# Performance work log

Hardware: AMD Instinct MI355X
Metric: run time of the kernel (lower is better)

## Reference

```python
import jax, jax.numpy as jnp
import numpy as np

B, T, D, H = 4, 1024, 1024, 16
DK = D // H
SCALE = float(np.sqrt(DK))


def setup_inputs() -> dict:
    key = jax.random.key(0)
    ks = jax.random.split(key, 12)
    std = 1.0 / np.sqrt(D)
    inp = {
        "x": jax.random.normal(ks[0], (B, T, D), dtype=jnp.float32),
        "s2_distances": jax.random.uniform(ks[1], (B, T, T), dtype=jnp.float32),
        # causal mask: 1 where attention allowed (j <= i)
        "mask": jnp.broadcast_to(jnp.tril(jnp.ones((T, T), dtype=jnp.int32)), (B, T, T)),
        "Wq": jax.random.uniform(ks[2], (D, D), jnp.float32, -std, std),
        "bq": jax.random.uniform(ks[3], (D,), jnp.float32, -std, std),
        "Wk": jax.random.uniform(ks[4], (D, D), jnp.float32, -std, std),
        "bk": jax.random.uniform(ks[5], (D,), jnp.float32, -std, std),
        "Wv": jax.random.uniform(ks[6], (D, D), jnp.float32, -std, std),
        "bv": jax.random.uniform(ks[7], (D,), jnp.float32, -std, std),
        "Wo": jax.random.uniform(ks[8], (D, D), jnp.float32, -std, std),
        "bo": jax.random.uniform(ks[9], (D,), jnp.float32, -std, std),
        "spatial_weight": jnp.float32(0.5),
    }
    return inp


def reference(x, s2_distances, mask, Wq, bq, Wk, bk, Wv, bv, Wo, bo, spatial_weight):
    b, t, _ = x.shape
    # projections: torch nn.Linear is x @ W.T + b
    def proj(W, bias):
        y = jnp.einsum("btd,ed->bte", x, W) + bias
        return y.reshape(b, t, H, DK).transpose(0, 2, 1, 3)  # [B,H,T,dk]

    Q, K, V = proj(Wq, bq), proj(Wk, bk), proj(Wv, bv)
    # scores: QK^T/sqrt(dk) - |alpha| * dist  (dist broadcast over heads)
    scores = jnp.einsum("bhqd,bhkd->bhqk", Q, K) / SCALE
    scores = scores - jnp.abs(spatial_weight) * s2_distances[:, None, :, :]
    scores = jnp.where(mask[:, None, :, :] == 0, -jnp.inf, scores)
    probs = jax.nn.softmax(scores, axis=-1)
    out = jnp.einsum("bhqk,bhkd->bhqd", probs, V)
    out = out.transpose(0, 2, 1, 3).reshape(b, t, D)
    return jnp.einsum("btd,ed->bte", out, Wo) + bo
```

## Files before the change

### kernel.cpp

```cpp
#include <hip/hip_runtime.h>
#include <stdint.h>

#define Tt 1024
#define Dd 1024
#define Hh 16

typedef unsigned short u16;
typedef __attribute__((ext_vector_type(8))) short short8;
typedef __attribute__((ext_vector_type(4))) float f32x4;
typedef __attribute__((ext_vector_type(4))) unsigned short u16x4;

typedef const __attribute__((address_space(1))) uint32_t* gptr_t;
typedef __attribute__((address_space(3))) uint32_t* lptr_t;

#define QSCALE 0.18033688011112042f
#define LOG2E 1.4426950408889634f

static __device__ __forceinline__ u16 f2bf(float f) {
  union { float f; unsigned u; } x;
  x.f = f;
  unsigned u = x.u;
  return (u16)((u + 0x7fffu + ((u >> 16) & 1u)) >> 16);
}

static __device__ __forceinline__ u16 f2bf_fast(float f) {
  union { float f; unsigned u; } x;
  x.f = f;
  return (u16)((x.u + 0x8000u) >> 16);
}

static __device__ __forceinline__ float fexp2(float x) {
#if __has_builtin(__builtin_amdgcn_exp2f)
  return __builtin_amdgcn_exp2f(x);
#else
  return exp2f(x);
#endif
}

__global__ __launch_bounds__(256) void cvt_kernel(
    const float* __restrict__ x, const float* __restrict__ wq,
    const float* __restrict__ wk, const float* __restrict__ wv,
    const float* __restrict__ wo, u16* __restrict__ xb, u16* __restrict__ wb) {
  size_t i = ((size_t)blockIdx.x * 256 + threadIdx.x) * 4;
  const size_t XN = (size_t)4 * 1024 * 1024;
  const float* src;
  u16* dst;
  size_t off;
  if (i < XN) {
    src = x; dst = xb; off = i;
  } else {
    size_t j = i - XN;
    int wi = (int)(j >> 20);
    src = (wi == 0) ? wq : (wi == 1) ? wk : (wi == 2) ? wv : wo;
    dst = wb + ((size_t)wi << 20);
    off = j & ((1u << 20) - 1);
  }
  float4 v = *(const float4*)(src + off);
  u16x4 o;
  o.x = f2bf(v.x); o.y = f2bf(v.y); o.z = f2bf(v.z); o.w = f2bf(v.w);
  *(u16x4*)(dst + off) = o;
}

static __device__ __forceinline__ void gemm_mainloop_db(
    const u16* __restrict__ A, const u16* __restrict__ W,
    u16* lds, int m0, int n0, f32x4 acc[2][4]) {
  const int t = threadIdx.x;
  const int w = t >> 6, l = t & 63;
  const int quad = l >> 4, l15 = l & 15;
  const int wm = (w >> 1) * 32, wn = (w & 1) * 64;
  const int srow = t >> 3;
  const int scol = ((l & 7) ^ ((l >> 3) & 7)) * 8;
  const u16* ga = A + (size_t)(m0 + srow) * Dd + scol;
  const u16* gb = W + (size_t)(n0 + srow) * Dd + scol;
  char* ldc = (char*)lds;
  const int xr = l15 & 7;

  auto stage = [&](int k0, int buf) {
    char* base = ldc + buf * 32768 + w * 1024;
#pragma unroll
    for (int i = 0; i < 2; i++) {
      __builtin_amdgcn_global_load_lds((gptr_t)(ga + k0 + (size_t)i * 64 * Dd),
                                       (lptr_t)(base + i * 8192), 16, 0, 0);
      __builtin_amdgcn_global_load_lds((gptr_t)(gb + k0 + (size_t)i * 64 * Dd),
                                       (lptr_t)(base + 16384 + i * 8192), 16, 0, 0);
    }
  };

  stage(0, 0);
#pragma unroll 1
  for (int it = 0; it < Dd / 64; it++) {
    const int buf = it & 1;
    __builtin_amdgcn_s_waitcnt(0);
    __syncthreads();
    if (it + 1 < Dd / 64) stage((it + 1) * 64, buf ^ 1);
    const u16* lA = lds + buf * 16384;
    const u16* lB = lA + 8192;
#pragma unroll
    for (int kk = 0; kk < 2; kk++) {
      short8 af[2], bfr[4];
#pragma unroll
      for (int mi = 0; mi < 2; mi++)
        af[mi] = *(const short8*)(lA + (wm + mi * 16 + l15) * 64 +
                                  (((kk * 4 + quad) ^ xr) * 8));
#pragma unroll
      for (int ni = 0; ni < 4; ni++)
        bfr[ni] = *(const short8*)(lB + (wn + ni * 16 + l15) * 64 +
                                   (((kk * 4 + quad) ^ xr) * 8));
#pragma unroll
      for (int mi = 0; mi < 2; mi++)
#pragma unroll
        for (int ni = 0; ni < 4; ni++)
          acc[mi][ni] = __builtin_amdgcn_mfma_f32_16x16x32_bf16(af[mi], bfr[ni], acc[mi][ni], 0, 0, 0);
    }
  }
}

__global__ __launch_bounds__(512) void gemm_qkv_kernel(
    const u16* __restrict__ xb, const u16* __restrict__ wb,
    const float* __restrict__ bq, const float* __restrict__ bk,
    const float* __restrict__ bv, u16* __restrict__ Q, u16* __restrict__ Kk,
    u16* __restrict__ Vt) {
  __shared__ u16 lds[2 * 16384];
  const int z = blockIdx.z;
  const u16* W = wb + ((size_t)z << 20);
  const float* bias = (z == 0) ? bq : (z == 1) ? bk : bv;
  const int m0 = blockIdx.x * 128, n0 = blockIdx.y * 128;
  f32x4 acc[2][4];
#pragma unroll
  for (int i = 0; i < 2; i++)
#pragma unroll
    for (int j = 0; j < 4; j++) acc[i][j] = (f32x4){0.f, 0.f, 0.f, 0.f};
  gemm_mainloop_db(xb, W, lds, m0, n0, acc);
  const int t = threadIdx.x, w = t >> 6, l = t & 63, quad = l >> 4, l15 = l & 15;
  const int wm = (w >> 1) * 32, wn = (w & 1) * 64;
  u16* smem = lds;
  __syncthreads();
  const float scl = (z == 0) ? QSCALE : 1.0f;
  if (z < 2) {
#pragma unroll
    for (int mi = 0; mi < 2; mi++)
#pragma unroll
      for (int ni = 0; ni < 4; ni++) {
        const int n = wn + ni * 16 + l15;
        const float bn = bias[n0 + n];
#pragma unroll
        for (int r = 0; r < 4; r++) {
          const int m = wm + mi * 16 + quad * 4 + r;
          smem[m * 128 + n] = f2bf((acc[mi][ni][r] + bn) * scl);
        }
      }
  } else {
#pragma unroll
    for (int mi = 0; mi < 2; mi++)
#pragma unroll
      for (int ni = 0; ni < 4; ni++) {
        const int n = wn + ni * 16 + l15;
        const float bn = bias[n0 + n];
        u16x4 o;
        o.x = f2bf(acc[mi][ni][0] + bn);
        o.y = f2bf(acc[mi][ni][1] + bn);
        o.z = f2bf(acc[mi][ni][2] + bn);
        o.w = f2bf(acc[mi][ni][3] + bn);
        *(u16x4*)&smem[n * 128 + wm + mi * 16 + quad * 4] = o;
      }
  }
  __syncthreads();
  const int row = t >> 4;
  const int col = (t & 15) * 8;
  if (z < 2) {
    u16* out = (z == 0) ? Q : Kk;
#pragma unroll
    for (int it = 0; it < 4; it++) {
      const int rr = it * 32 + row;
      *(short8*)(out + (size_t)(m0 + rr) * Dd + n0 + col) = *(const short8*)&smem[rr * 128 + col];
    }
  } else {
    const int b2 = m0 >> 10, tt0 = m0 & (Tt - 1);
#pragma unroll
    for (int it = 0; it < 4; it++) {
      const int rr = it * 32 + row;
      *(short8*)(Vt + ((size_t)b2 * Dd + n0 + rr) * Tt + tt0 + col) = *(const short8*)&smem[rr * 128 + col];
    }
  }
}

__global__ __launch_bounds__(512) void gemm_out_kernel(
    const u16* __restrict__ Ao, const u16* __restrict__ Wo,
    const float* __restrict__ bo, float* __restrict__ out) {
  __shared__ u16 lds[2 * 16384];
  const int m0 = blockIdx.x * 128, n0 = blockIdx.y * 128;
  f32x4 acc[2][4];
#pragma unroll
  for (int i = 0; i < 2; i++)
#pragma unroll
    for (int j = 0; j < 4; j++) acc[i][j] = (f32x4){0.f, 0.f, 0.f, 0.f};
  gemm_mainloop_db(Ao, Wo, lds, m0, n0, acc);
  const int t = threadIdx.x, w = t >> 6, l = t & 63, quad = l >> 4, l15 = l & 15;
  const int wm = (w >> 1) * 32, wn = (w & 1) * 64;
#pragma unroll
  for (int mi = 0; mi < 2; mi++)
#pragma unroll
    for (int ni = 0; ni < 4; ni++) {
      const int n = n0 + wn + ni * 16 + l15;
      const float bn = bo[n];
#pragma unroll
      for (int r = 0; r < 4; r++) {
        const int m = m0 + wm + mi * 16 + quad * 4 + r;
        out[(size_t)m * Dd + n] = acc[mi][ni][r] + bn;
      }
    }
}

__global__ __launch_bounds__(256) void attn_kernel(
    const u16* __restrict__ Q, const u16* __restrict__ Kk,
    const u16* __restrict__ Vt, const float* __restrict__ dist,
    const float* __restrict__ alphap, u16* __restrict__ Oo) {
  __shared__ u16 lK[2][64 * 64];
  __shared__ u16 lV[2][64 * 64];
  __shared__ u16 lPp[4][16 * 64];
  const int t = threadIdx.x, w = t >> 6, l = t & 63, quad = l >> 4, l15 = l & 15;
  const int pi = blockIdx.x & 7;
  const int bh = blockIdx.x >> 3;
  const int h = bh & (Hh - 1), b = bh >> 4;
  const int qbA = pi, qbB = 15 - pi;
  const float aL = fabsf(alphap[0]) * LOG2E;
  const float* distb = dist + (size_t)b * Tt * Tt;

  const int srow = w * 8 + (l >> 3);
  const int schunk = ((l & 7) ^ ((l >> 3) & 7)) * 8;
  const u16* gK = Kk + ((size_t)b * Tt + srow) * Dd + h * 64 + schunk;
  const u16* gV = Vt + ((size_t)b * Dd + h * 64 + srow) * Tt + schunk;
  char* lKc0 = (char*)&lK[0][0];
  char* lVc0 = (char*)&lV[0][0];
  const int wbase = w * 1024;

  auto stage = [&](int k0, int buf) {
#pragma unroll
    for (int i = 0; i < 2; i++) {
      __builtin_amdgcn_global_load_lds(
          (gptr_t)(gK + (size_t)(k0 + i * 32) * Dd),
          (lptr_t)(lKc0 + buf * 8192 + wbase + i * 4096), 16, 0, 0);
      __builtin_amdgcn_global_load_lds(
          (gptr_t)(gV + (size_t)(i * 32) * Tt + k0),
          (lptr_t)(lVc0 + buf * 8192 + wbase + i * 4096), 16, 0, 0);
    }
  };

  const int qrowA = qbA * 64 + w * 16 + l15;
  const int qrowB = qbB * 64 + w * 16 + l15;
  const u16* QpA = Q + ((size_t)b * Tt + qrowA) * Dd + h * 64 + quad * 8;
  const u16* QpB = Q + ((size_t)b * Tt + qrowB) * Dd + h * 64 + quad * 8;
  const short8 qfA0 = *(const short8*)QpA;
  const short8 qfA1 = *(const short8*)(QpA + 32);
  const short8 qfB0 = *(const short8*)QpB;
  const short8 qfB1 = *(const short8*)(QpB + 32);
  const float* dpA = distb + (size_t)qrowA * Tt + quad * 4;
  const float* dpB = distb + (size_t)qrowB * Tt + quad * 4;

  const int xr = l15 & 7;
  u16* lpr = &lPp[w][l15 * 64];

  f32x4 ddA[4], ddB[4];
  stage(0, 0);
#pragma unroll
  for (int nt = 0; nt < 4; nt++) ddA[nt] = *(const f32x4*)(dpA + nt * 16);

  int gi = 0;
#pragma unroll 1
  for (int half = 0; half < 2; half++) {
    const int qb = half ? qbB : qbA;
    const int q0 = qb * 64;
    const int niter = qb + 1;
    const short8 qf0 = half ? qfB0 : qfA0;
    const short8 qf1 = half ? qfB1 : qfA1;
    const float* dp = half ? dpB : dpA;
    const int qrow = half ? qrowB : qrowA;
    f32x4 oacc[4];
#pragma unroll
    for (int dt = 0; dt < 4; dt++) oacc[dt] = (f32x4){0.f, 0.f, 0.f, 0.f};
    float lsum = 0.f;

#pragma unroll 1
    for (int kt = 0; kt < niter; kt++, gi++) {
      const int buf = gi & 1;
      __builtin_amdgcn_s_waitcnt(0);
      __syncthreads();
      const bool more = (kt + 1 < niter);
      if (more) {
        stage((kt + 1) * 64, buf ^ 1);
#pragma unroll
        for (int nt = 0; nt < 4; nt++)
          ddB[nt] = *(const f32x4*)(dp + (kt + 1) * 64 + nt * 16);
      } else if (half == 0) {
        stage(0, buf ^ 1);
#pragma unroll
        for (int nt = 0; nt < 4; nt++) ddB[nt] = *(const f32x4*)(dpB + nt * 16);
      }
      f32x4 sacc[4];
#pragma unroll
      for (int nt = 0; nt < 4; nt++) {
#pragma unroll
        for (int r = 0; r < 4; r++) sacc[nt][r] = -aL * ddA[nt][r];
      }
#pragma unroll
      for (int ks = 0; ks < 2; ks++) {
        const short8 qf = ks ? qf1 : qf0;
        const int cs = ((ks * 4 + quad) ^ xr) * 8;
#pragma unroll
        for (int nt = 0; nt < 4; nt++) {
          const short8 kf = *(const short8*)&lK[buf][(nt * 16 + l15) * 64 + cs];
          sacc[nt] = __builtin_amdgcn_mfma_f32_16x16x32_bf16(kf, qf, sacc[nt], 0, 0, 0);
        }
      }
      if (kt == qb) {
        const int kbase = kt * 64 + quad * 4;
#pragma unroll
        for (int nt = 0; nt < 4; nt++) {
          u16x4 pk;
#pragma unroll
          for (int r = 0; r < 4; r++) {
            const float p = (kbase + nt * 16 + r <= qrow) ? fexp2(sacc[nt][r]) : 0.f;
            lsum += p;
            pk[r] = f2bf_fast(p);
          }
          *(u16x4*)&lpr[((nt * 4 + quad) ^ (xr << 1)) * 4] = pk;
        }
      } else {
#pragma unroll
        for (int nt = 0; nt < 4; nt++) {
          u16x4 pk;
#pragma unroll
          for (int r = 0; r < 4; r++) {
            const float p = fexp2(sacc[nt][r]);
            lsum += p;
            pk[r] = f2bf_fast(p);
          }
          *(u16x4*)&lpr[((nt * 4 + quad) ^ (xr << 1)) * 4] = pk;
        }
      }
#pragma unroll
      for (int ks = 0; ks < 2; ks++) {
        const short8 pa = *(const short8*)&lpr[((ks * 4 + quad) ^ xr) * 8];
        const int cs = ((ks * 4 + quad) ^ xr) * 8;
#pragma unroll
        for (int dt = 0; dt < 4; dt++) {
          const short8 vf = *(const short8*)&lV[buf][(dt * 16 + l15) * 64 + cs];
          oacc[dt] = __builtin_amdgcn_mfma_f32_16x16x32_bf16(pa, vf, oacc[dt], 0, 0, 0);
        }
      }
#pragma unroll
      for (int nt = 0; nt < 4; nt++) ddA[nt] = ddB[nt];
    }

    lsum += __shfl_xor(lsum, 16);
    lsum += __shfl_xor(lsum, 32);
    const float inv = 1.0f / lsum;
    float invq[4];
#pragma unroll
    for (int r = 0; r < 4; r++) invq[r] = __shfl(inv, quad * 4 + r);
#pragma unroll
    for (int dt = 0; dt < 4; dt++) {
#pragma unroll
      for (int r = 0; r < 4; r++) {
        Oo[((size_t)b * Tt + q0 + w * 16 + quad * 4 + r) * Dd + h * 64 + dt * 16 + l15] =
            f2bf(oacc[dt][r] * invq[r]);
      }
    }
  }
}

extern "C" void kernel_launch(void* const* d_in, const int* in_sizes, int n_in,
                              void* d_out, int out_size, void* d_ws, size_t ws_size,
                              hipStream_t stream) {
  const float* x = (const float*)d_in[0];
  const float* dist = (const float*)d_in[1];
  const float* Wq = (const float*)d_in[3];
  const float* bq = (const float*)d_in[4];
  const float* Wk = (const float*)d_in[5];
  const float* bk = (const float*)d_in[6];
  const float* Wv = (const float*)d_in[7];
  const float* bv = (const float*)d_in[8];
  const float* Wo = (const float*)d_in[9];
  const float* bo = (const float*)d_in[10];
  const float* alphap = (const float*)d_in[11];

  char* ws = (char*)d_ws;
  u16* xb = (u16*)(ws);
  u16* wb = (u16*)(ws + ((size_t)8 << 20));
  u16* Qb = (u16*)(ws + ((size_t)16 << 20));
  u16* Kb = (u16*)(ws + ((size_t)24 << 20));
  u16* Vtb = (u16*)(ws + ((size_t)32 << 20));
  u16* Ob = xb;
  float* outp = (float*)d_out;

  cvt_kernel<<<8192, 256, 0, stream>>>(x, Wq, Wk, Wv, Wo, xb, wb);
  dim3 g1(32, 8, 3);
  gemm_qkv_kernel<<<g1, 512, 0, stream>>>(xb, wb, bq, bk, bv, Qb, Kb, Vtb);
  attn_kernel<<<512, 256, 0, stream>>>(Qb, Kb, Vtb, dist, alphap, Ob);
  dim3 g2(32, 8);
  gemm_out_kernel<<<g2, 512, 0, stream>>>(Ob, wb + ((size_t)3 << 20), bo, outp);
}
```

Baseline: 196.6 us.

## Prescale distance bias to bf16, split attention blocks per q-tile, narrow out-proj tiles

The convert kernel now also turns the full distance matrix into a bf16 bias already multiplied by -|alpha|*log2e, so the attention kernel streams half as many bytes and skips the per-element multiply. The attention grid changes from paired q-blocks (balanced causal work) to one q-block per workgroup, with the largest blocks dispatched first, doubling the block count. The output projection uses 128x64 tiles with its own inline mainloop, giving twice as many blocks for better CU fill. The cost is an extra full read and write of the distance matrix in the convert pass, plus bf16 rounding of the bias.

After: 197.0 us. About the same (+0.2%).

```diff
diff --git a/kernel.cpp b/kernel.cpp
--- a/kernel.cpp
+++ b/kernel.cpp
@@ -27,6 +27,12 @@
   union { float f; unsigned u; } x;
   x.f = f;
   return (u16)((x.u + 0x8000u) >> 16);
+}
+
+static __device__ __forceinline__ float bf2f(u16 u) {
+  union { unsigned u; float f; } x;
+  x.u = ((unsigned)u) << 16;
+  return x.f;
 }
 
 static __device__ __forceinline__ float fexp2(float x) {
@@ -40,24 +46,32 @@
 __global__ __launch_bounds__(256) void cvt_kernel(
     const float* __restrict__ x, const float* __restrict__ wq,
     const float* __restrict__ wk, const float* __restrict__ wv,
-    const float* __restrict__ wo, u16* __restrict__ xb, u16* __restrict__ wb) {
+    const float* __restrict__ wo, const float* __restrict__ dist,
+    const float* __restrict__ alphap, u16* __restrict__ xb,
+    u16* __restrict__ wb, u16* __restrict__ biasb) {
   size_t i = ((size_t)blockIdx.x * 256 + threadIdx.x) * 4;
   const size_t XN = (size_t)4 * 1024 * 1024;
+  const size_t WN = (size_t)4 * 1024 * 1024;
+  float scl = 1.0f;
   const float* src;
   u16* dst;
   size_t off;
   if (i < XN) {
     src = x; dst = xb; off = i;
-  } else {
+  } else if (i < XN + WN) {
     size_t j = i - XN;
     int wi = (int)(j >> 20);
     src = (wi == 0) ? wq : (wi == 1) ? wk : (wi == 2) ? wv : wo;
     dst = wb + ((size_t)wi << 20);
     off = j & ((1u << 20) - 1);
+  } else {
+    src = dist; dst = biasb; off = i - XN - WN;
+    scl = -fabsf(alphap[0]) * LOG2E;
   }
   float4 v = *(const float4*)(src + off);
   u16x4 o;
-  o.x = f2bf(v.x); o.y = f2bf(v.y); o.z = f2bf(v.z); o.w = f2bf(v.w);
+  o.x = f2bf(v.x * scl); o.y = f2bf(v.y * scl);
+  o.z = f2bf(v.z * scl); o.w = f2bf(v.w * scl);
   *(u16x4*)(dst + off) = o;
 }
 
@@ -187,44 +201,73 @@
 __global__ __launch_bounds__(512) void gemm_out_kernel(
     const u16* __restrict__ Ao, const u16* __restrict__ Wo,
     const float* __restrict__ bo, float* __restrict__ out) {
-  __shared__ u16 lds[2 * 16384];
-  const int m0 = blockIdx.x * 128, n0 = blockIdx.y * 128;
-  f32x4 acc[2][4];
-#pragma unroll
-  for (int i = 0; i < 2; i++)
-#pragma unroll
-    for (int j = 0; j < 4; j++) acc[i][j] = (f32x4){0.f, 0.f, 0.f, 0.f};
-  gemm_mainloop_db(Ao, Wo, lds, m0, n0, acc);
+  __shared__ u16 lds[2 * 12288];
+  const int m0 = blockIdx.x * 128, n0 = blockIdx.y * 64;
   const int t = threadIdx.x, w = t >> 6, l = t & 63, quad = l >> 4, l15 = l & 15;
-  const int wm = (w >> 1) * 32, wn = (w & 1) * 64;
-#pragma unroll
-  for (int mi = 0; mi < 2; mi++)
-#pragma unroll
-    for (int ni = 0; ni < 4; ni++) {
-      const int n = n0 + wn + ni * 16 + l15;
-      const float bn = bo[n];
-#pragma unroll
-      for (int r = 0; r < 4; r++) {
-        const int m = m0 + wm + mi * 16 + quad * 4 + r;
-        out[(size_t)m * Dd + n] = acc[mi][ni][r] + bn;
-      }
-    }
+  const int srow = t >> 3;
+  const int scol = ((l & 7) ^ ((l >> 3) & 7)) * 8;
+  const u16* ga = Ao + (size_t)(m0 + srow) * Dd + scol;
+  const u16* gb = Wo + (size_t)(n0 + srow) * Dd + scol;
+  char* ldc = (char*)lds;
+  const int xr = l15 & 7;
+  f32x4 acc[4];
+#pragma unroll
+  for (int j = 0; j < 4; j++) acc[j] = (f32x4){0.f, 0.f, 0.f, 0.f};
+
+  auto stage = [&](int k0, int buf) {
+    char* base = ldc + buf * 24576 + w * 1024;
+#pragma unroll
+    for (int i = 0; i < 2; i++)
+      __builtin_amdgcn_global_load_lds((gptr_t)(ga + k0 + (size_t)i * 64 * Dd),
+                                       (lptr_t)(base + i * 8192), 16, 0, 0);
+    __builtin_amdgcn_global_load_lds((gptr_t)(gb + k0),
+                                     (lptr_t)(base + 16384), 16, 0, 0);
+  };
+
+  stage(0, 0);
+#pragma unroll 1
+  for (int it = 0; it < Dd / 64; it++) {
+    const int buf = it & 1;
+    __builtin_amdgcn_s_waitcnt(0);
+    __syncthreads();
+    if (it + 1 < Dd / 64) stage((it + 1) * 64, buf ^ 1);
+    const u16* lA = lds + buf * 12288;
+    const u16* lB = lA + 8192;
+#pragma unroll
+    for (int kk = 0; kk < 2; kk++) {
+      const int cs = ((kk * 4 + quad) ^ xr) * 8;
+      const short8 af = *(const short8*)(lA + (w * 16 + l15) * 64 + cs);
+#pragma unroll
+      for (int ni = 0; ni < 4; ni++) {
+        const short8 bfr = *(const short8*)(lB + (ni * 16 + l15) * 64 + cs);
+        acc[ni] = __builtin_amdgcn_mfma_f32_16x16x32_bf16(af, bfr, acc[ni], 0, 0, 0);
+      }
+    }
+  }
+#pragma unroll
+  for (int ni = 0; ni < 4; ni++) {
+    const int n = n0 + ni * 16 + l15;
+    const float bn = bo[n];
+#pragma unroll
+    for (int r = 0; r < 4; r++) {
+      const int m = m0 + w * 16 + quad * 4 + r;
+      out[(size_t)m * Dd + n] = acc[ni][r] + bn;
+    }
+  }
 }
 
 __global__ __launch_bounds__(256) void attn_kernel(
     const u16* __restrict__ Q, const u16* __restrict__ Kk,
-    const u16* __restrict__ Vt, const float* __restrict__ dist,
-    const float* __restrict__ alphap, u16* __restrict__ Oo) {
+    const u16* __restrict__ Vt, const u16* __restrict__ biasb,
+    u16* __restrict__ Oo) {
   __shared__ u16 lK[2][64 * 64];
   __shared__ u16 lV[2][64 * 64];
   __shared__ u16 lPp[4][16 * 64];
   const int t = threadIdx.x, w = t >> 6, l = t & 63, quad = l >> 4, l15 = l & 15;
-  const int pi = blockIdx.x & 7;
-  const int bh = blockIdx.x >> 3;
+  const int qb = 15 - (blockIdx.x >> 6);
+  const int bh = blockIdx.x & 63;
   const int h = bh & (Hh - 1), b = bh >> 4;
-  const int qbA = pi, qbB = 15 - pi;
-  const float aL = fabsf(alphap[0]) * LOG2E;
-  const float* distb = dist + (size_t)b * Tt * Tt;
+  const int q0 = qb * 64;
 
   const int srow = w * 8 + (l >> 3);
   const int schunk = ((l & 7) ^ ((l >> 3) & 7)) * 8;
@@ -246,125 +289,105 @@
     }
   };
 
-  const int qrowA = qbA * 64 + w * 16 + l15;
-  const int qrowB = qbB * 64 + w * 16 + l15;
-  const u16* QpA = Q + ((size_t)b * Tt + qrowA) * Dd + h * 64 + quad * 8;
-  const u16* QpB = Q + ((size_t)b * Tt + qrowB) * Dd + h * 64 + quad * 8;
-  const short8 qfA0 = *(const short8*)QpA;
-  const short8 qfA1 = *(const short8*)(QpA + 32);
-  const short8 qfB0 = *(const short8*)QpB;
-  const short8 qfB1 = *(const short8*)(QpB + 32);
-  const float* dpA = distb + (size_t)qrowA * Tt + quad * 4;
-  const float* dpB = distb + (size_t)qrowB * Tt + quad * 4;
+  const int qrow = q0 + w * 16 + l15;
+  const u16* Qp = Q + ((size_t)b * Tt + qrow) * Dd + h * 64 + quad * 8;
+  const short8 qf0 = *(const short8*)Qp;
+  const short8 qf1 = *(const short8*)(Qp + 32);
+  const u16* bp = biasb + ((size_t)b * Tt + qrow) * Tt + quad * 4;
 
   const int xr = l15 & 7;
   u16* lpr = &lPp[w][l15 * 64];
-
-  f32x4 ddA[4], ddB[4];
+  const int niter = qb + 1;
+
+  f32x4 oacc[4];
+#pragma unroll
+  for (int dt = 0; dt < 4; dt++) oacc[dt] = (f32x4){0.f, 0.f, 0.f, 0.f};
+  float lsum = 0.f;
+  u16x4 bbA[4], bbB[4];
+
   stage(0, 0);
 #pragma unroll
-  for (int nt = 0; nt < 4; nt++) ddA[nt] = *(const f32x4*)(dpA + nt * 16);
-
-  int gi = 0;
+  for (int nt = 0; nt < 4; nt++) bbA[nt] = *(const u16x4*)(bp + nt * 16);
+
 #pragma unroll 1
-  for (int half = 0; half < 2; half++) {
-    const int qb = half ? qbB : qbA;
-    const int q0 = qb * 64;
-    const int niter = qb + 1;
-    const short8 qf0 = half ? qfB0 : qfA0;
-    const short8 qf1 = half ? qfB1 : qfA1;
-    const float* dp = half ? dpB : dpA;
-    const int qrow = half ? qrowB : qrowA;
-    f32x4 oacc[4];
-#pragma unroll
-    for (int dt = 0; dt < 4; dt++) oacc[dt] = (f32x4){0.f, 0.f, 0.f, 0.f};
-    float lsum = 0.f;
-
-#pragma unroll 1
-    for (int kt = 0; kt < niter; kt++, gi++) {
-      const int buf = gi & 1;
-      __builtin_amdgcn_s_waitcnt(0);
-      __syncthreads();
-      const bool more = (kt + 1 < niter);
-      if (more) {
-        stage((kt + 1) * 64, buf ^ 1);
-#pragma unroll
-        for (int nt = 0; nt < 4; nt++)
-          ddB[nt] = *(const f32x4*)(dp + (kt + 1) * 64 + nt * 16);
-      } else if (half == 0) {
-        stage(0, buf ^ 1);
-#pragma unroll
-        for (int nt = 0; nt < 4; nt++) ddB[nt] = *(const f32x4*)(dpB + nt * 16);
-      }
-      f32x4 sacc[4];
+  for (int kt = 0; kt < niter; kt++) {
+    const int buf = kt & 1;
+    __builtin_amdgcn_s_waitcnt(0);
+    __syncthreads();
+    if (kt + 1 < niter) {
+      stage((kt + 1) * 64, buf ^ 1);
+#pragma unroll
+      for (int nt = 0; nt < 4; nt++)
+        bbB[nt] = *(const u16x4*)(bp + (kt + 1) * 64 + nt * 16);
+    }
+    f32x4 sacc[4];
+#pragma unroll
+    for (int nt = 0; nt < 4; nt++) {
+#pragma unroll
+      for (int r = 0; r < 4; r++) sacc[nt][r] = bf2f(bbA[nt][r]);
+    }
+#pragma unroll
+    for (int ks = 0; ks < 2; ks++) {
+      const short8 qf = ks ? qf1 : qf0;
+      const int cs = ((ks * 4 + quad) ^ xr) * 8;
 #pragma unroll
       for (int nt = 0; nt < 4; nt++) {
-#pragma unroll
-        for (int r = 0; r < 4; r++) sacc[nt][r] = -aL * ddA[nt][r];
-      }
-#pragma unroll
-      for (int ks = 0; ks < 2; ks++) {
-        const short8 qf = ks ? qf1 : qf0;
-        const int cs = ((ks * 4 + quad) ^ xr) * 8;
-#pragma unroll
-        for (int nt = 0; nt < 4; nt++) {
-          const short8 kf = *(const short8*)&lK[buf][(nt * 16 + l15) * 64 + cs];
-          sacc[nt] = __builtin_amdgcn_mfma_f32_16x16x32_bf16(kf, qf, sacc[nt], 0, 0, 0);
+        const short8 kf = *(const short8*)&lK[buf][(nt * 16 + l15) * 64 + cs];
+        sacc[nt] = __builtin_amdgcn_mfma_f32_16x16x32_bf16(kf, qf, sacc[nt], 0, 0, 0);
+      }
+    }
+    if (kt == qb) {
+      const int kbase = kt * 64 + quad * 4;
+#pragma unroll
+      for (int nt = 0; nt < 4; nt++) {
+        u16x4 pk;
+#pragma unroll
+        for (int r = 0; r < 4; r++) {
+          const float p = (kbase + nt * 16 + r <= qrow) ? fexp2(sacc[nt][r]) : 0.f;
+          lsum += p;
+          pk[r] = f2bf_fast(p);
         }
-      }
-      if (kt == qb) {
-        const int kbase = kt * 64 + quad * 4;
-#pragma unroll
-        for (int nt = 0; nt < 4; nt++) {
-          u16x4 pk;
-#pragma unroll
-          for (int r = 0; r < 4; r++) {
-            const float p = (kbase + nt * 16 + r <= qrow) ? fexp2(sacc[nt][r]) : 0.f;
-            lsum += p;
-            pk[r] = f2bf_fast(p);
-          }
-          *(u16x4*)&lpr[((nt * 4 + quad) ^ (xr << 1)) * 4] = pk;
+        *(u16x4*)&lpr[((nt * 4 + quad) ^ (xr << 1)) * 4] = pk;
+      }
+    } else {
+#pragma unroll
+      for (int nt = 0; nt < 4; nt++) {
+        u16x4 pk;
+#pragma unroll
+        for (int r = 0; r < 4; r++) {
+          const float p = fexp2(sacc[nt][r]);
+          lsum += p;
+          pk[r] = f2bf_fast(p);
         }
-      } else {
-#pragma unroll
-        for (int nt = 0; nt < 4; nt++) {
-          u16x4 pk;
-#pragma unroll
-          for (int r = 0; r < 4; r++) {
-            const float p = fexp2(sacc[nt][r]);
-            lsum += p;
-            pk[r] = f2bf_fast(p);
-          }
-          *(u16x4*)&lpr[((nt * 4 + quad) ^ (xr << 1)) * 4] = pk;
-        }
-      }
-#pragma unroll
-      for (int ks = 0; ks < 2; ks++) {
-        const short8 pa = *(const short8*)&lpr[((ks * 4 + quad) ^ xr) * 8];
-        const int cs = ((ks * 4 + quad) ^ xr) * 8;
-#pragma unroll
-        for (int dt = 0; dt < 4; dt++) {
-          const short8 vf = *(const short8*)&lV[buf][(dt * 16 + l15) * 64 + cs];
-          oacc[dt] = __builtin_amdgcn_mfma_f32_16x16x32_bf16(pa, vf, oacc[dt], 0, 0, 0);
-        }
-      }
-#pragma unroll
-      for (int nt = 0; nt < 4; nt++) ddA[nt] = ddB[nt];
-    }
-
-    lsum += __shfl_xor(lsum, 16);
-    lsum += __shfl_xor(lsum, 32);
-    const float inv = 1.0f / lsum;
-    float invq[4];
-#pragma unroll
-    for (int r = 0; r < 4; r++) invq[r] = __shfl(inv, quad * 4 + r);
-#pragma unroll
-    for (int dt = 0; dt < 4; dt++) {
-#pragma unroll
-      for (int r = 0; r < 4; r++) {
-        Oo[((size_t)b * Tt + q0 + w * 16 + quad * 4 + r) * Dd + h * 64 + dt * 16 + l15] =
-            f2bf(oacc[dt][r] * invq[r]);
-      }
+        *(u16x4*)&lpr[((nt * 4 + quad) ^ (xr << 1)) * 4] = pk;
+      }
+    }
+#pragma unroll
+    for (int ks = 0; ks < 2; ks++) {
+      const int cs = ((ks * 4 + quad) ^ xr) * 8;
+      const short8 pa = *(const short8*)&lpr[cs];
+#pragma unroll
+      for (int dt = 0; dt < 4; dt++) {
+        const short8 vf = *(const short8*)&lV[buf][(dt * 16 + l15) * 64 + cs];
+        oacc[dt] = __builtin_amdgcn_mfma_f32_16x16x32_bf16(pa, vf, oacc[dt], 0, 0, 0);
+      }
+    }
+#pragma unroll
+    for (int nt = 0; nt < 4; nt++) bbA[nt] = bbB[nt];
+  }
+
+  lsum += __shfl_xor(lsum, 16);
+  lsum += __shfl_xor(lsum, 32);
+  const float inv = 1.0f / lsum;
+  float invq[4];
+#pragma unroll
+  for (int r = 0; r < 4; r++) invq[r] = __shfl(inv, quad * 4 + r);
+#pragma unroll
+  for (int dt = 0; dt < 4; dt++) {
+#pragma unroll
+    for (int r = 0; r < 4; r++) {
+      Oo[((size_t)b * Tt + q0 + w * 16 + quad * 4 + r) * Dd + h * 64 + dt * 16 + l15] =
+          f2bf(oacc[dt][r] * invq[r]);
     }
   }
 }
@@ -390,13 +413,14 @@
   u16* Qb = (u16*)(ws + ((size_t)16 << 20));
   u16* Kb = (u16*)(ws + ((size_t)24 << 20));
   u16* Vtb = (u16*)(ws + ((size_t)32 << 20));
+  u16* biasb = (u16*)(ws + ((size_t)40 << 20));
   u16* Ob = xb;
   float* outp = (float*)d_out;
 
-  cvt_kernel<<<8192, 256, 0, stream>>>(x, Wq, Wk, Wv, Wo, xb, wb);
+  cvt_kernel<<<12288, 256, 0, stream>>>(x, Wq, Wk, Wv, Wo, dist, alphap, xb, wb, biasb);
   dim3 g1(32, 8, 3);
   gemm_qkv_kernel<<<g1, 512, 0, stream>>>(xb, wb, bq, bk, bv, Qb, Kb, Vtb);
-  attn_kernel<<<512, 256, 0, stream>>>(Qb, Kb, Vtb, dist, alphap, Ob);
-  dim3 g2(32, 8);
+  attn_kernel<<<1024, 256, 0, stream>>>(Qb, Kb, Vtb, biasb, Ob);
+  dim3 g2(32, 16);
   gemm_out_kernel<<<g2, 512, 0, stream>>>(Ob, wb + ((size_t)3 << 20), bo, outp);
 }
```
